# Performance work log

Measured on AMD Instinct MI355X. Metric: run time of the kernel, lower is better.

Reference implementation:

```python
import jax, jax.numpy as jnp
import numpy as np

B, N, C = 8, 2048, 512  # batch, points, channels; dk == C


def _mlp(x, W, b):
    # torch MLP helper = Linear followed by ReLU (even on the last layer)
    return jax.nn.relu(x @ W + b)


def setup_inputs() -> dict:
    key = jax.random.key(0)
    ks = jax.random.split(key, 5)
    s = 1.0 / np.sqrt(C)
    return {
        "x": jax.random.normal(ks[0], (B, N, C), dtype=jnp.float32),
        "Wh": jax.random.normal(ks[1], (C, C), dtype=jnp.float32) * s,
        "bh": jnp.zeros((C,), dtype=jnp.float32),
        "Wl": jax.random.normal(ks[2], (C, C), dtype=jnp.float32) * s,
        "bl": jnp.zeros((C,), dtype=jnp.float32),
        "Wg": jax.random.normal(ks[3], (C, C), dtype=jnp.float32) * s,
        "bg": jnp.zeros((C,), dtype=jnp.float32),
        "Wm": jax.random.normal(ks[4], (C, C), dtype=jnp.float32) * s,
        "bm": jnp.zeros((C,), dtype=jnp.float32),
    }


def reference(x, Wh, bh, Wl, bl, Wg, bg, Wm, bm):
    h = _mlp(x, Wh, bh)                      # [B, N, dk] (torch transposes; folded into einsum)
    l = _mlp(x, Wl, bl)                      # [B, N, dk]
    scores = jnp.einsum("bnd,bmd->bnm", l, h)  # [B, N, N]
    attn = jax.nn.softmax(scores, axis=-1)
    g = _mlp(x, Wg, bg)                      # [B, N, C]
    out = x + jnp.einsum("bnm,bmc->bnc", attn, g)
    return _mlp(out, Wm, bm)
```

## Files before the change

### kernel.cpp

```cpp
#include <hip/hip_runtime.h>


typedef __attribute__((ext_vector_type(4))) float f32x4;
typedef __attribute__((ext_vector_type(8))) short s16x8;
typedef __attribute__((ext_vector_type(4))) short s16x4;
typedef __attribute__((ext_vector_type(8))) _Float16 f16x8;
typedef __attribute__((ext_vector_type(4))) _Float16 f16x4;
typedef __attribute__((ext_vector_type(2))) unsigned u32x2;

typedef unsigned int u32;
typedef __attribute__((address_space(1))) const u32 gu32;
typedef __attribute__((address_space(3))) u32 lu32;

__device__ __forceinline__ void gload16(const short* g, short* l) {
  __builtin_amdgcn_global_load_lds((gu32*)g, (lu32*)l, 16, 0, 0);
}

__device__ __forceinline__ short f2h(float f) {
  _Float16 h = (_Float16)f;
  return __builtin_bit_cast(short, h);
}

__device__ __forceinline__ unsigned pk2h(float a, float b) {
  return __builtin_bit_cast(unsigned, __builtin_amdgcn_cvt_pkrtz(a, b));
}

#define MFMA(a, b, c) __builtin_amdgcn_mfma_f32_16x16x32_f16(a, b, c, 0, 0, 0)
#define MFMA16(a, b, c) __builtin_amdgcn_mfma_f32_16x16x16f16(a, b, c, 0, 0, 0)

#define BAR_KEEP2()                                          \
  do {                                                       \
    asm volatile("s_waitcnt vmcnt(2)" ::: "memory");         \
    __builtin_amdgcn_s_barrier();                            \
    __builtin_amdgcn_sched_barrier(0);                       \
  } while (0)
#define BAR_KEEP2_L()                                        \
  do {                                                       \
    asm volatile("s_waitcnt vmcnt(2) lgkmcnt(0)" ::: "memory"); \
    __builtin_amdgcn_s_barrier();                            \
    __builtin_amdgcn_sched_barrier(0);                       \
  } while (0)
#define BAR_KEEP4_L()                                        \
  do {                                                       \
    asm volatile("s_waitcnt vmcnt(4) lgkmcnt(0)" ::: "memory"); \
    __builtin_amdgcn_s_barrier();                            \
    __builtin_amdgcn_sched_barrier(0);                       \
  } while (0)
#define BAR_VM0()                                            \
  do {                                                       \
    asm volatile("s_waitcnt vmcnt(0)" ::: "memory");         \
    __builtin_amdgcn_s_barrier();                            \
    __builtin_amdgcn_sched_barrier(0);                       \
  } while (0)
#define BAR_ALL()                                            \
  do {                                                       \
    asm volatile("s_waitcnt vmcnt(0) lgkmcnt(0)" ::: "memory"); \
    __builtin_amdgcn_s_barrier();                            \
    __builtin_amdgcn_sched_barrier(0);                       \
  } while (0)


__global__ __launch_bounds__(256) void conv_w_kernel(const float* __restrict__ Wh,
                                                     const float* __restrict__ Wl,
                                                     const float* __restrict__ Wg,
                                                     const float* __restrict__ Wm,
                                                     short* __restrict__ Wt) {
  __shared__ float lds[64][65];
  int w = blockIdx.x >> 6, tile = blockIdx.x & 63;
  int tk = (tile >> 3) * 64, tn = (tile & 7) * 64;
  const float* W = (w == 0) ? Wh : (w == 1) ? Wl : (w == 2) ? Wg : Wm;
  int tid = threadIdx.x;

  int rr = tid >> 4, cc4 = (tid & 15) * 4;
#pragma unroll
  for (int p = 0; p < 4; ++p) {
    int row = rr + p * 16;
    float4 v = *(const float4*)&W[(size_t)(tk + row) * 512 + tn + cc4];
    lds[row][cc4] = v.x; lds[row][cc4 + 1] = v.y;
    lds[row][cc4 + 2] = v.z; lds[row][cc4 + 3] = v.w;
  }
  __syncthreads();

  int k8 = (tid & 7) * 8;
#pragma unroll
  for (int p = 0; p < 2; ++p) {
    int n = (tid >> 3) + p * 32;
    s16x8 o;
#pragma unroll
    for (int j = 0; j < 8; ++j) o[j] = f2h(lds[k8 + j][n]);
    *(s16x8*)&Wt[(size_t)w * 262144 + (size_t)(tn + n) * 512 + tk + k8] = o;
  }
}


__global__ __launch_bounds__(256) void mlp3_kernel(const float* __restrict__ x,
                                                   const short* __restrict__ Wt_all,
                                                   const float* __restrict__ bh,
                                                   const float* __restrict__ bl,
                                                   const float* __restrict__ bg,
                                                   short* __restrict__ h,
                                                   short* __restrict__ l,
                                                   short* __restrict__ gT) {
  int z = blockIdx.z;
  const short* Wt = Wt_all + z * 262144;
  const float* bias = (z == 0) ? bh : (z == 1) ? bl : bg;

  __shared__ __align__(16) short abuf[2][4096];
  __shared__ __align__(16) short bbuf[3][4096];
  int tid = threadIdx.x, lane = tid & 63, w = tid >> 6;
  int wm = w >> 1, wn = w & 1;
  int bm = blockIdx.x * 128, bn = blockIdx.y * 128;
  int rx = lane & 15, g = lane >> 4;

  auto stageB = [&](int t) {
    int k0 = t * 32;
    short* bd = &bbuf[t % 3][0];
    int srow = lane >> 2;
    int scol = ((lane & 3) ^ ((lane >> 3) & 3)) * 8;
#pragma unroll
    for (int j = 0; j < 2; ++j) {
      int wl = w * 2 + j;
      int row = wl * 16 + srow;
      gload16(Wt + (size_t)(bn + row) * 512 + k0 + scol, bd + wl * 512 + lane * 8);
    }
  };
  auto loadA = [&](int t, s16x8 av[2]) {
#pragma unroll
    for (int it = 0; it < 2; ++it) {
      int c = tid + it * 256;
      int row = c >> 2, col8 = (c & 3) * 8;
      size_t base = (size_t)(bm + row) * 512 + t * 32 + col8;
      float4 x0 = *(const float4*)&x[base];
      float4 x1 = *(const float4*)&x[base + 4];
      s16x8 v;
      v[0] = f2h(x0.x); v[1] = f2h(x0.y); v[2] = f2h(x0.z); v[3] = f2h(x0.w);
      v[4] = f2h(x1.x); v[5] = f2h(x1.y); v[6] = f2h(x1.z); v[7] = f2h(x1.w);
      av[it] = v;
    }
  };
  auto writeA = [&](int t, s16x8 av[2]) {
    short* ad = &abuf[t & 1][0];
#pragma unroll
    for (int it = 0; it < 2; ++it) {
      int c = tid + it * 256;
      int row = c >> 2;
      int chunk_p = (c & 3) ^ ((row >> 1) & 3);
      *(s16x8*)&ad[row * 32 + chunk_p * 8] = av[it];
    }
  };

  f32x4 acc[4][4];
#pragma unroll
  for (int mi = 0; mi < 4; ++mi)
#pragma unroll
    for (int ni = 0; ni < 4; ++ni) acc[mi][ni] = (f32x4){0.f, 0.f, 0.f, 0.f};

  s16x8 av[2];
  loadA(0, av);
  stageB(0); stageB(1);
  writeA(0, av);
  BAR_KEEP2_L();

  int foff = rx * 32 + ((g ^ ((rx >> 1) & 3)) << 3);

  for (int t = 0; t < 16; ++t) {
    if (t < 15) loadA(t + 1, av);
    if (t < 14) stageB(t + 2);
    const short* ab = &abuf[t & 1][0];
    const short* bb = &bbuf[t % 3][0];
    f16x8 af[4], bfr[4];
#pragma unroll
    for (int mi = 0; mi < 4; ++mi)
      af[mi] = *(const f16x8*)&ab[(wm * 64 + mi * 16) * 32 + foff];
#pragma unroll
    for (int ni = 0; ni < 4; ++ni)
      bfr[ni] = *(const f16x8*)&bb[(wn * 64 + ni * 16) * 32 + foff];
#pragma unroll
    for (int mi = 0; mi < 4; ++mi)
#pragma unroll
      for (int ni = 0; ni < 4; ++ni) acc[mi][ni] = MFMA(af[mi], bfr[ni], acc[mi][ni]);
    if (t < 15) writeA(t + 1, av);
    if (t < 14) BAR_KEEP2_L();
    else if (t == 14) BAR_ALL();
  }

#pragma unroll
  for (int mi = 0; mi < 4; ++mi)
#pragma unroll
    for (int ni = 0; ni < 4; ++ni) {
      int col = bn + wn * 64 + ni * 16 + rx;
      float bv = bias[col];
#pragma unroll
      for (int r = 0; r < 4; ++r) {
        int row = bm + wm * 64 + mi * 16 + g * 4 + r;
        float v = fmaxf(acc[mi][ni][r] + bv, 0.0f);
        short o = f2h(v);
        if (z == 0) h[(size_t)row * 512 + col] = o;
        else if (z == 1) l[(size_t)row * 512 + col] = o;
        else {
          int bb2 = row >> 11, mm = row & 2047;
          gT[((size_t)bb2 * 512 + col) * 2048 + mm] = o;
        }
      }
    }
}


__global__ __launch_bounds__(512, 1) void attn_split_kernel(
    const short* __restrict__ lmat, const short* __restrict__ hmat,
    const short* __restrict__ gT,
    short* __restrict__ OA, short* __restrict__ OB,
    float2* __restrict__ mlA, float2* __restrict__ mlB) {
  __shared__ __align__(16) short kbuf[3][8192];
  __shared__ __align__(16) short gbuf[2][8192];
  int tid = threadIdx.x, lane = tid & 63, w = tid >> 6;
  int b = blockIdx.x & 7;
  int idx = blockIdx.x >> 3;
  int qt = idx >> 1, sp = idx & 1;
  int q0 = qt * 128 + w * 16;
  int keybase = sp * 1024;
  const short* lb = lmat + (size_t)b * 2048 * 512;
  const short* hb = hmat + (size_t)b * 2048 * 512;
  const short* gb = gT + (size_t)b * 512 * 2048;
  short* Op = sp ? OB : OA;
  float2* ml = sp ? mlB : mlA;

  int r0 = lane & 15, g = lane >> 4;

  f16x8 qf[16];
  {
    int q = q0 + r0;
#pragma unroll
    for (int ks = 0; ks < 16; ++ks)
      qf[ks] = *(const f16x8*)&lb[(size_t)q * 512 + ks * 32 + g * 8];
  }
  f32x4 accO[32];
#pragma unroll
  for (int i = 0; i < 32; ++i) accO[i] = (f32x4){0.f, 0.f, 0.f, 0.f};
  float mrun = -3e38f, lsumL = 0.f;

  auto stageK = [&](int t) {
    int key0 = keybase + t * 16;
    short* kd = &kbuf[t % 3][0];
#pragma unroll
    for (int j = 0; j < 2; ++j) {
      int wl = w * 2 + j;
      gload16(hb + (size_t)(key0 + wl) * 512 + (((lane * 16) ^ ((wl & 7) << 4)) >> 1),
              kd + wl * 512);
    }
  };
  auto stageG = [&](int t) {
    int key0 = keybase + t * 16;
    short* gd = &gbuf[t & 1][0];
#pragma unroll
    for (int j = 0; j < 2; ++j) {
      int wl = w * 2 + j;
      int c = wl * 32 + (lane >> 1);
      int half = (lane & 1) ^ ((lane >> 3) & 1);
      gload16(gb + (size_t)c * 2048 + key0 + half * 8, gd + wl * 512);
    }
  };
  auto QK = [&](int t, f32x4& o) {
    const short* kb = &kbuf[t % 3][0];
#pragma unroll
    for (int ks = 0; ks < 16; ++ks) {
      f16x8 kf = *(const f16x8*)&kb[(r0 * 512 + ks * 32 + g * 8) ^ ((r0 & 7) << 3)];
      o = MFMA(kf, qf[ks], o);
    }
  };

  stageK(0); stageK(1); stageG(0); stageK(2);
  BAR_KEEP2();
  f32x4 sc = {0.f, 0.f, 0.f, 0.f};
  QK(0, sc);
  BAR_KEEP2();

  int goff = r0 * 16 + (((g >> 1) ^ ((r0 >> 2) & 1)) << 3) + ((g & 1) << 2);

  for (int t = 0; t < 64; ++t) {
    if (t < 63) stageG(t + 1);
    if (t < 61) stageK(t + 3);

    f32x4 sn = {0.f, 0.f, 0.f, 0.f};
    if (t < 63) {
      __builtin_amdgcn_s_setprio(1);
      QK(t + 1, sn);
      __builtin_amdgcn_s_setprio(0);
    }

    float m2 = fmaxf(fmaxf(sc[0], sc[1]), fmaxf(sc[2], sc[3]));
    m2 = fmaxf(m2, __shfl_xor(m2, 16));
    m2 = fmaxf(m2, __shfl_xor(m2, 32));
    bool ok = (m2 <= mrun + 8.0f);
    if (!__all((int)ok)) {
      float mnew = fmaxf(mrun, m2);
      float s = __expf(mrun - mnew);
      mrun = mnew;
      lsumL *= s;
#pragma unroll
      for (int nf = 0; nf < 32; ++nf) accO[nf] *= s;
    }
    float p0 = __expf(sc[0] - mrun), p1 = __expf(sc[1] - mrun);
    float p2 = __expf(sc[2] - mrun), p3 = __expf(sc[3] - mrun);
    lsumL += (p0 + p1) + (p2 + p3);

    u32x2 pw = {pk2h(p0, p1), pk2h(p2, p3)};
    f16x4 pfrag = __builtin_bit_cast(f16x4, pw);

    const short* gp = &gbuf[t & 1][goff];
    __builtin_amdgcn_s_setprio(1);
#pragma unroll
    for (int nf = 0; nf < 32; ++nf) {
      f16x4 gf = *(const f16x4*)&gp[nf * 256];
      accO[nf] = MFMA16(gf, pfrag, accO[nf]);
    }
    __builtin_amdgcn_s_setprio(0);

    if (t < 61) BAR_KEEP2(); else BAR_VM0();
    sc = sn;
  }

  float ls = lsumL;
  ls += __shfl_xor(ls, 16);
  ls += __shfl_xor(ls, 32);
  float inv = 1.0f / ls;
  int q = q0 + r0;
#pragma unroll
  for (int nf = 0; nf < 32; ++nf) {
    s16x4 o;
    o[0] = f2h(accO[nf][0] * inv);
    o[1] = f2h(accO[nf][1] * inv);
    o[2] = f2h(accO[nf][2] * inv);
    o[3] = f2h(accO[nf][3] * inv);
    *(s16x4*)&Op[((size_t)b * 2048 + q) * 512 + nf * 16 + g * 4] = o;
  }
  if (g == 0) ml[(size_t)b * 2048 + q] = make_float2(mrun, ls);
}


__global__ __launch_bounds__(256) void final_gemm_kernel(
    const short* __restrict__ OA, const short* __restrict__ OB,
    const float2* __restrict__ mlA, const float2* __restrict__ mlB,
    const float* __restrict__ x, const short* __restrict__ Wt,
    const float* __restrict__ bias, float* __restrict__ out) {
  __shared__ __align__(16) short abuf[2][4096];
  __shared__ __align__(16) short bbuf[3][4096];
  int tid = threadIdx.x, lane = tid & 63, w = tid >> 6;
  int wm = w >> 1, wn = w & 1;
  int bm = blockIdx.x * 128, bn = blockIdx.y * 128;
  int rx = lane & 15, g = lane >> 4;

  float wgt[2][2];
#pragma unroll
  for (int it = 0; it < 2; ++it) {
    int row = (tid >> 2) + it * 64;
    float2 a2 = mlA[bm + row], b2 = mlB[bm + row];
    float ms = fmaxf(a2.x, b2.x);
    float wA = __expf(a2.x - ms) * a2.y;
    float wB = __expf(b2.x - ms) * b2.y;
    float winv = 1.0f / (wA + wB);
    wgt[it][0] = wA * winv;
    wgt[it][1] = wB * winv;
  }

  auto stageB = [&](int t) {
    int k0 = t * 32;
    short* bd = &bbuf[t % 3][0];
    int srow = lane >> 2;
    int scol = ((lane & 3) ^ ((lane >> 3) & 3)) * 8;
#pragma unroll
    for (int j = 0; j < 2; ++j) {
      int wl = w * 2 + j;
      int row = wl * 16 + srow;
      gload16(Wt + (size_t)(bn + row) * 512 + k0 + scol, bd + wl * 512 + lane * 8);
    }
  };
  auto loadA = [&](int t, s16x8 av[2]) {
#pragma unroll
    for (int it = 0; it < 2; ++it) {
      int c = tid + it * 256;
      int row = c >> 2, col8 = (c & 3) * 8;
      size_t base = (size_t)(bm + row) * 512 + t * 32 + col8;
      f16x8 oa = *(const f16x8*)&OA[base];
      f16x8 ob = *(const f16x8*)&OB[base];
      float4 x0 = *(const float4*)&x[base];
      float4 x1 = *(const float4*)&x[base + 4];
      float wA = wgt[it][0], wB = wgt[it][1];
      s16x8 v;
      v[0] = f2h((float)oa[0] * wA + (float)ob[0] * wB + x0.x);
      v[1] = f2h((float)oa[1] * wA + (float)ob[1] * wB + x0.y);
      v[2] = f2h((float)oa[2] * wA + (float)ob[2] * wB + x0.z);
      v[3] = f2h((float)oa[3] * wA + (float)ob[3] * wB + x0.w);
      v[4] = f2h((float)oa[4] * wA + (float)ob[4] * wB + x1.x);
      v[5] = f2h((float)oa[5] * wA + (float)ob[5] * wB + x1.y);
      v[6] = f2h((float)oa[6] * wA + (float)ob[6] * wB + x1.z);
      v[7] = f2h((float)oa[7] * wA + (float)ob[7] * wB + x1.w);
      av[it] = v;
    }
  };
  auto writeA = [&](int t, s16x8 av[2]) {
    short* ad = &abuf[t & 1][0];
#pragma unroll
    for (int it = 0; it < 2; ++it) {
      int c = tid + it * 256;
      int row = c >> 2;
      int chunk_p = (c & 3) ^ ((row >> 1) & 3);
      *(s16x8*)&ad[row * 32 + chunk_p * 8] = av[it];
    }
  };

  f32x4 acc[4][4];
#pragma unroll
  for (int mi = 0; mi < 4; ++mi)
#pragma unroll
    for (int ni = 0; ni < 4; ++ni) acc[mi][ni] = (f32x4){0.f, 0.f, 0.f, 0.f};

  s16x8 av[2];
  loadA(0, av);
  stageB(0); stageB(1);
  writeA(0, av);
  BAR_KEEP4_L();

  int foff = rx * 32 + ((g ^ ((rx >> 1) & 3)) << 3);

  for (int t = 0; t < 16; ++t) {
    if (t < 15) loadA(t + 1, av);
    if (t < 14) stageB(t + 2);
    const short* ab = &abuf[t & 1][0];
    const short* bb = &bbuf[t % 3][0];
    f16x8 af[4], bfr[4];
#pragma unroll
    for (int mi = 0; mi < 4; ++mi)
      af[mi] = *(const f16x8*)&ab[(wm * 64 + mi * 16) * 32 + foff];
#pragma unroll
    for (int ni = 0; ni < 4; ++ni)
      bfr[ni] = *(const f16x8*)&bb[(wn * 64 + ni * 16) * 32 + foff];
#pragma unroll
    for (int mi = 0; mi < 4; ++mi)
#pragma unroll
      for (int ni = 0; ni < 4; ++ni) acc[mi][ni] = MFMA(af[mi], bfr[ni], acc[mi][ni]);
    if (t < 15) writeA(t + 1, av);
    if (t < 14) BAR_KEEP4_L();
    else if (t == 14) BAR_ALL();
  }

#pragma unroll
  for (int mi = 0; mi < 4; ++mi)
#pragma unroll
    for (int ni = 0; ni < 4; ++ni) {
      int col = bn + wn * 64 + ni * 16 + rx;
      float bv = bias[col];
#pragma unroll
      for (int r = 0; r < 4; ++r) {
        int row = bm + wm * 64 + mi * 16 + g * 4 + r;
        out[(size_t)row * 512 + col] = fmaxf(acc[mi][ni][r] + bv, 0.0f);
      }
    }
}


extern "C" void kernel_launch(void* const* d_in, const int* in_sizes, int n_in,
                              void* d_out, int out_size, void* d_ws, size_t ws_size,
                              hipStream_t stream) {
  const float* x  = (const float*)d_in[0];
  const float* Wh = (const float*)d_in[1];
  const float* bh = (const float*)d_in[2];
  const float* Wl = (const float*)d_in[3];
  const float* bl = (const float*)d_in[4];
  const float* Wg = (const float*)d_in[5];
  const float* bg = (const float*)d_in[6];
  const float* Wm = (const float*)d_in[7];
  const float* bm = (const float*)d_in[8];

  char* ws = (char*)d_ws;
  const size_t SZ = 16777216;
  short*  OA  = (short*)(ws + 0 * SZ);
  short*  h   = (short*)(ws + 1 * SZ);
  short*  l   = (short*)(ws + 2 * SZ);
  short*  gT  = (short*)(ws + 3 * SZ);
  short*  OB  = (short*)(ws + 4 * SZ);
  short*  Wt  = (short*)(ws + 5 * SZ);
  float2* mlA = (float2*)(ws + 5 * SZ + 2097152);
  float2* mlB = (float2*)(ws + 5 * SZ + 2097152 + 131072);

  conv_w_kernel<<<256, 256, 0, stream>>>(Wh, Wl, Wg, Wm, Wt);
  mlp3_kernel<<<dim3(128, 4, 3), 256, 0, stream>>>(x, Wt, bh, bl, bg, h, l, gT);
  attn_split_kernel<<<256, 512, 0, stream>>>(l, h, gT, OA, OB, mlA, mlB);
  final_gemm_kernel<<<dim3(128, 4), 256, 0, stream>>>(OA, OB, mlA, mlB, x,
                                                      Wt + 3 * 262144, bm,
                                                      (float*)d_out);
}
```

Baseline: 230.4 us.

## Pair warps to split head dim in attention, exchanging partial scores via LDS

```diff
diff --git a/kernel.cpp b/kernel.cpp
--- a/kernel.cpp
+++ b/kernel.cpp
@@ -46,9 +46,9 @@
     __builtin_amdgcn_s_barrier();                            \
     __builtin_amdgcn_sched_barrier(0);                       \
   } while (0)
-#define BAR_VM0()                                            \
+#define BAR_VM0_L()                                          \
   do {                                                       \
-    asm volatile("s_waitcnt vmcnt(0)" ::: "memory");         \
+    asm volatile("s_waitcnt vmcnt(0) lgkmcnt(0)" ::: "memory"); \
     __builtin_amdgcn_s_barrier();                            \
     __builtin_amdgcn_sched_barrier(0);                       \
   } while (0)
@@ -213,11 +213,14 @@
     float2* __restrict__ mlA, float2* __restrict__ mlB) {
   __shared__ __align__(16) short kbuf[3][8192];
   __shared__ __align__(16) short gbuf[2][8192];
+  __shared__ __align__(16) f32x4 sbuf[2][8][2][64];
   int tid = threadIdx.x, lane = tid & 63, w = tid >> 6;
   int b = blockIdx.x & 7;
   int idx = blockIdx.x >> 3;
   int qt = idx >> 1, sp = idx & 1;
-  int q0 = qt * 128 + w * 16;
+  int p = w >> 1, dh = w & 1;
+  int q0 = qt * 128 + p * 32;
+  int dbase = dh * 256;
   int keybase = sp * 1024;
   const short* lb = lmat + (size_t)b * 2048 * 512;
   const short* hb = hmat + (size_t)b * 2048 * 512;
@@ -226,18 +229,21 @@
   float2* ml = sp ? mlB : mlA;
 
   int r0 = lane & 15, g = lane >> 4;
-
-  f16x8 qf[16];
-  {
-    int q = q0 + r0;
-#pragma unroll
-    for (int ks = 0; ks < 16; ++ks)
-      qf[ks] = *(const f16x8*)&lb[(size_t)q * 512 + ks * 32 + g * 8];
-  }
-  f32x4 accO[32];
-#pragma unroll
-  for (int i = 0; i < 32; ++i) accO[i] = (f32x4){0.f, 0.f, 0.f, 0.f};
-  float mrun = -3e38f, lsumL = 0.f;
+  int qA = q0 + r0, qB = q0 + 16 + r0;
+
+  f16x8 qf[8][2];
+#pragma unroll
+  for (int kc = 0; kc < 8; ++kc) {
+    qf[kc][0] = *(const f16x8*)&lb[(size_t)qA * 512 + dbase + kc * 32 + g * 8];
+    qf[kc][1] = *(const f16x8*)&lb[(size_t)qB * 512 + dbase + kc * 32 + g * 8];
+  }
+  f32x4 accO[16][2];
+#pragma unroll
+  for (int i = 0; i < 16; ++i) {
+    accO[i][0] = (f32x4){0.f, 0.f, 0.f, 0.f};
+    accO[i][1] = (f32x4){0.f, 0.f, 0.f, 0.f};
+  }
+  float mrA = -3e38f, mrB = -3e38f, lsA = 0.f, lsB = 0.f;
 
   auto stageK = [&](int t) {
     int key0 = keybase + t * 16;
@@ -260,81 +266,98 @@
       gload16(gb + (size_t)c * 2048 + key0 + half * 8, gd + wl * 512);
     }
   };
-  auto QK = [&](int t, f32x4& o) {
+  auto QKp = [&](int t) {
     const short* kb = &kbuf[t % 3][0];
-#pragma unroll
-    for (int ks = 0; ks < 16; ++ks) {
-      f16x8 kf = *(const f16x8*)&kb[(r0 * 512 + ks * 32 + g * 8) ^ ((r0 & 7) << 3)];
-      o = MFMA(kf, qf[ks], o);
-    }
+    f32x4 s0 = {0.f, 0.f, 0.f, 0.f}, s1 = {0.f, 0.f, 0.f, 0.f};
+#pragma unroll
+    for (int kc = 0; kc < 8; ++kc) {
+      f16x8 kf = *(const f16x8*)&kb[(r0 * 512 + dbase + kc * 32 + g * 8) ^
+                                    ((r0 & 7) << 3)];
+      s0 = MFMA(kf, qf[kc][0], s0);
+      s1 = MFMA(kf, qf[kc][1], s1);
+    }
+    sbuf[t & 1][w][0][lane] = s0;
+    sbuf[t & 1][w][1][lane] = s1;
   };
 
   stageK(0); stageK(1); stageG(0); stageK(2);
   BAR_KEEP2();
-  f32x4 sc = {0.f, 0.f, 0.f, 0.f};
-  QK(0, sc);
-  BAR_KEEP2();
-
-  int goff = r0 * 16 + (((g >> 1) ^ ((r0 >> 2) & 1)) << 3) + ((g & 1) << 2);
+  __builtin_amdgcn_s_setprio(1);
+  QKp(0);
+  __builtin_amdgcn_s_setprio(0);
+  BAR_KEEP2_L();
+
+  int goff = (dbase + r0) * 16 + (((g >> 1) ^ ((r0 >> 2) & 1)) << 3) + ((g & 1) << 2);
 
   for (int t = 0; t < 64; ++t) {
     if (t < 63) stageG(t + 1);
     if (t < 61) stageK(t + 3);
 
-    f32x4 sn = {0.f, 0.f, 0.f, 0.f};
     if (t < 63) {
       __builtin_amdgcn_s_setprio(1);
-      QK(t + 1, sn);
+      QKp(t + 1);
       __builtin_amdgcn_s_setprio(0);
     }
 
-    float m2 = fmaxf(fmaxf(sc[0], sc[1]), fmaxf(sc[2], sc[3]));
-    m2 = fmaxf(m2, __shfl_xor(m2, 16));
-    m2 = fmaxf(m2, __shfl_xor(m2, 32));
-    bool ok = (m2 <= mrun + 8.0f);
+    f32x4 o0 = sbuf[t & 1][w][0][lane] + sbuf[t & 1][w ^ 1][0][lane];
+    f32x4 o1 = sbuf[t & 1][w][1][lane] + sbuf[t & 1][w ^ 1][1][lane];
+
+    float mA = fmaxf(fmaxf(o0[0], o0[1]), fmaxf(o0[2], o0[3]));
+    float mB = fmaxf(fmaxf(o1[0], o1[1]), fmaxf(o1[2], o1[3]));
+    mA = fmaxf(mA, __shfl_xor(mA, 16)); mA = fmaxf(mA, __shfl_xor(mA, 32));
+    mB = fmaxf(mB, __shfl_xor(mB, 16)); mB = fmaxf(mB, __shfl_xor(mB, 32));
+    bool ok = (mA <= mrA + 8.0f) && (mB <= mrB + 8.0f);
     if (!__all((int)ok)) {
-      float mnew = fmaxf(mrun, m2);
-      float s = __expf(mrun - mnew);
-      mrun = mnew;
-      lsumL *= s;
-#pragma unroll
-      for (int nf = 0; nf < 32; ++nf) accO[nf] *= s;
-    }
-    float p0 = __expf(sc[0] - mrun), p1 = __expf(sc[1] - mrun);
-    float p2 = __expf(sc[2] - mrun), p3 = __expf(sc[3] - mrun);
-    lsumL += (p0 + p1) + (p2 + p3);
-
-    u32x2 pw = {pk2h(p0, p1), pk2h(p2, p3)};
-    f16x4 pfrag = __builtin_bit_cast(f16x4, pw);
+      float nA = fmaxf(mrA, mA), nB = fmaxf(mrB, mB);
+      float sA = __expf(mrA - nA), sB = __expf(mrB - nB);
+      mrA = nA; mrB = nB;
+      lsA *= sA; lsB *= sB;
+#pragma unroll
+      for (int nf = 0; nf < 16; ++nf) { accO[nf][0] *= sA; accO[nf][1] *= sB; }
+    }
+    float a0 = __expf(o0[0] - mrA), a1 = __expf(o0[1] - mrA);
+    float a2 = __expf(o0[2] - mrA), a3 = __expf(o0[3] - mrA);
+    float b0 = __expf(o1[0] - mrB), b1 = __expf(o1[1] - mrB);
+    float b2 = __expf(o1[2] - mrB), b3 = __expf(o1[3] - mrB);
+    lsA += (a0 + a1) + (a2 + a3);
+    lsB += (b0 + b1) + (b2 + b3);
+
+    u32x2 pwA = {pk2h(a0, a1), pk2h(a2, a3)};
+    u32x2 pwB = {pk2h(b0, b1), pk2h(b2, b3)};
+    f16x4 pfA = __builtin_bit_cast(f16x4, pwA);
+    f16x4 pfB = __builtin_bit_cast(f16x4, pwB);
 
     const short* gp = &gbuf[t & 1][goff];
     __builtin_amdgcn_s_setprio(1);
 #pragma unroll
-    for (int nf = 0; nf < 32; ++nf) {
+    for (int nf = 0; nf < 16; ++nf) {
       f16x4 gf = *(const f16x4*)&gp[nf * 256];
-      accO[nf] = MFMA16(gf, pfrag, accO[nf]);
+      accO[nf][0] = MFMA16(gf, pfA, accO[nf][0]);
+      accO[nf][1] = MFMA16(gf, pfB, accO[nf][1]);
     }
     __builtin_amdgcn_s_setprio(0);
 
-    if (t < 61) BAR_KEEP2(); else BAR_VM0();
-    sc = sn;
-  }
-
-  float ls = lsumL;
-  ls += __shfl_xor(ls, 16);
-  ls += __shfl_xor(ls, 32);
-  float inv = 1.0f / ls;
-  int q = q0 + r0;
-#pragma unroll
-  for (int nf = 0; nf < 32; ++nf) {
-    s16x4 o;
-    o[0] = f2h(accO[nf][0] * inv);
-    o[1] = f2h(accO[nf][1] * inv);
-    o[2] = f2h(accO[nf][2] * inv);
-    o[3] = f2h(accO[nf][3] * inv);
-    *(s16x4*)&Op[((size_t)b * 2048 + q) * 512 + nf * 16 + g * 4] = o;
-  }
-  if (g == 0) ml[(size_t)b * 2048 + q] = make_float2(mrun, ls);
+    if (t < 61) BAR_KEEP2_L(); else BAR_VM0_L();
+  }
+
+  lsA += __shfl_xor(lsA, 16); lsA += __shfl_xor(lsA, 32);
+  lsB += __shfl_xor(lsB, 16); lsB += __shfl_xor(lsB, 32);
+  float invA = 1.0f / lsA, invB = 1.0f / lsB;
+#pragma unroll
+  for (int nf = 0; nf < 16; ++nf) {
+    int col = dbase + nf * 16 + g * 4;
+    s16x4 oA4, oB4;
+    oA4[0] = f2h(accO[nf][0][0] * invA); oA4[1] = f2h(accO[nf][0][1] * invA);
+    oA4[2] = f2h(accO[nf][0][2] * invA); oA4[3] = f2h(accO[nf][0][3] * invA);
+    oB4[0] = f2h(accO[nf][1][0] * invB); oB4[1] = f2h(accO[nf][1][1] * invB);
+    oB4[2] = f2h(accO[nf][1][2] * invB); oB4[3] = f2h(accO[nf][1][3] * invB);
+    *(s16x4*)&Op[((size_t)b * 2048 + qA) * 512 + col] = oA4;
+    *(s16x4*)&Op[((size_t)b * 2048 + qB) * 512 + col] = oB4;
+  }
+  if (dh == 0 && g == 0) {
+    ml[(size_t)b * 2048 + qA] = make_float2(mrA, lsA);
+    ml[(size_t)b * 2048 + qB] = make_float2(mrB, lsB);
+  }
 }
 
 
```

Result: slower. 243.3 us (+5.6%).
